# Kernel optimization log

Hardware: AMD Instinct MI355X
Metric: run time of the kernel (lower is better)

The kernel has to match this reference:

```python
import jax, jax.numpy as jnp
import numpy as np

K1 = 3                      # spline kernel size per pseudo dim
SIZE = float(np.sqrt(2.0))  # pseudo_cartesian normalization size


def spline_weights(p, k):
    """Degree-1 open B-spline basis over 2D pseudo coords.
    p: [..., 2] in [0,1]. Returns basis [..., 4], weight_index [..., 4]."""
    v = jnp.clip(p, 0.0, 1.0) * (k - 1)
    lo = jnp.floor(v)
    frac = v - lo
    lo = lo.astype(jnp.int32)
    off = jnp.array([0, 1], dtype=jnp.int32)
    w0 = jnp.stack([1.0 - frac[..., 0], frac[..., 0]], axis=-1)   # [...,2]
    w1 = jnp.stack([1.0 - frac[..., 1], frac[..., 1]], axis=-1)   # [...,2]
    i0 = jnp.clip(lo[..., 0:1] + off, 0, k - 1)                    # [...,2]
    i1 = jnp.clip(lo[..., 1:2] + off, 0, k - 1)                    # [...,2]
    basis = (w0[..., :, None] * w1[..., None, :]).reshape(*p.shape[:-1], 4)
    widx = (i0[..., :, None] + k * i1[..., None, :]).reshape(*p.shape[:-1], 4)
    return basis, widx


def setup_inputs() -> dict:
    key = jax.random.key(0)
    kx, ke, kp, kq, kw, kb = jax.random.split(key, 6)
    N, C, P, E, K = 50000, 64, 16, 800000, K1 * K1
    x = jax.random.normal(kx, (N, C), dtype=jnp.float32)
    pos = jax.random.uniform(kp, (N, 2), dtype=jnp.float32)
    pose = jax.random.normal(kq, (N, P, 2), dtype=jnp.float32)
    pose = pose / (jnp.linalg.norm(pose, axis=-1, keepdims=True) + 1e-8)  # unit pose vectors
    W = jax.random.normal(kw, (P, K, C), dtype=jnp.float32) / np.sqrt(C * 4.0)
    bias = jax.random.normal(kb, (P,), dtype=jnp.float32) * 0.01
    edge_index = jax.random.randint(ke, (2, E), 0, N, dtype=jnp.int64)
    return {"x": x, "pos": pos, "pose": pose, "W": W, "bias": bias,
            "edge_index": edge_index}


def reference(x, pos, pose, W, bias, edge_index):
    N, C = x.shape
    P = pose.shape[1]
    row, col = edge_index[0], edge_index[1]
    # pseudo_cartesian: normalized relative position in [0,1]^2
    pseudo = (pos[col] - pos[row]) / (2.0 * SIZE) + 0.5              # [E,2]
    # posevec_to_rotmat on detached pose vectors
    pose_c = jax.lax.stop_gradient(pose)
    a, b = pose_c[..., 0], pose_c[..., 1]
    R = jnp.stack([jnp.stack([a, -b], -1), jnp.stack([b, a], -1)], -2)  # [N,P,2,2]
    Re = R[row]                                                      # [E,P,2,2]
    # rotate pseudo coords about (0.5, 0.5), batched over all poses
    p = jnp.einsum('epij,ej->epi', Re, pseudo - 0.5) + 0.5           # [E,P,2]
    basis, widx = spline_weights(p, K1)                              # [E,P,4]
    # SplineConv (out_channels=1, no root weight, no norm):
    # precompute per-node per-pose per-kernel-bin projections
    Z = jnp.einsum('nc,pkc->npk', x, W)                              # [N,P,K]
    pidx = jnp.arange(P)[None, :, None]
    vals = Z[col[:, None, None], pidx, widx]                         # [E,P,4]
    msg = jnp.sum(basis * vals, axis=-1)                             # [E,P]
    out = jax.ops.segment_sum(msg, row, num_segments=N)              # [N,P]
    return out + bias[None, :]
```

## Files before the change

kernel.cpp:

```cpp
#include <hip/hip_runtime.h>

#define C_DIM 64
#define P_DIM 16
#define K_DIM 9
#define ZROW 10
#define ZNODE (P_DIM * ZROW)
#define NT 10
#define WELEM (160 * C_DIM)
#define INV2S 0.35355339059327373f

typedef __attribute__((ext_vector_type(8))) short short8v;
typedef __attribute__((ext_vector_type(4))) float f32x4;
typedef uint uint4a __attribute__((ext_vector_type(4), aligned(4)));

__device__ __forceinline__ ushort f2bf(float f) {
    uint u = __builtin_bit_cast(uint, f);
    return (ushort)((u + 0x7FFFu + ((u >> 16) & 1u)) >> 16);
}
__device__ __forceinline__ float bf2f(ushort h) {
    return __builtin_bit_cast(float, ((uint)h) << 16);
}

__global__ __launch_bounds__(256) void prep_kernel(const float* __restrict__ W,
                                                   const float* __restrict__ pose,
                                                   const float* __restrict__ bias,
                                                   float* __restrict__ out,
                                                   ushort* __restrict__ Whi,
                                                   ushort* __restrict__ Wlo,
                                                   uint* __restrict__ pose_bf,
                                                   int N) {
    const int g = blockIdx.x * 256 + threadIdx.x;
    const int gsz = gridDim.x * 256;

    if (g < WELEM / 2) {
        const int j  = g >> 5;
        const int k2 = g & 31;
        const int p  = j / 10;
        const int k  = j - p * 10;
        float2 w2 = make_float2(0.0f, 0.0f);
        if (k < 9) w2 = ((const float2*)W)[(p * 9 + k) * (C_DIM / 2) + k2];
        const ushort h0 = f2bf(w2.x);
        const ushort h1 = f2bf(w2.y);
        ((uint*)Whi)[g] = (uint)h0 | ((uint)h1 << 16);
        ((uint*)Wlo)[g] = (uint)f2bf(w2.x - bf2f(h0)) |
                          ((uint)f2bf(w2.y - bf2f(h1)) << 16);
    }

    if (pose_bf != nullptr) {
        for (int i = g; i < N * P_DIM; i += gsz) {
            const float2 ab = ((const float2*)pose)[i];
            pose_bf[i] = (uint)f2bf(ab.x) | ((uint)f2bf(ab.y) << 16);
        }
    }

    {
        const float4 b4 = ((const float4*)bias)[g & 3];
        for (int i = g; i < N * 4; i += gsz) ((float4*)out)[i] = b4;
    }
}

__global__ __launch_bounds__(256) void z_gemm_kernel(const float* __restrict__ x,
                                                     const ushort* __restrict__ Whi,
                                                     const ushort* __restrict__ Wlo,
                                                     ushort* __restrict__ Zb,
                                                     int N) {
    __shared__ ushort w_hi[WELEM];
    __shared__ ushort w_lo[WELEM];

    const int tid = threadIdx.x;
    const int block_row = blockIdx.x * 64;

    for (int i = tid; i < 160 * 16; i += 256) {
        const uint4 vh = ((const uint4*)Whi)[i];
        const uint4 vl = ((const uint4*)Wlo)[i];
        const int lin = i * 8;
        const int j   = lin >> 6;
        const int w   = lin & 63;
        const int swz = j * 64 + (w ^ ((j & 7) << 3));
        *(uint4*)&w_hi[swz] = vh;
        *(uint4*)&w_lo[swz] = vl;
    }
    __syncthreads();

    const int lane = tid & 63;
    const int wv   = tid >> 6;
    const int col  = lane & 15;
    const int kg   = lane >> 4;

    const int arow = block_row + wv * 16 + col;
    const float* xr = x + (size_t)(arow < N ? arow : 0) * C_DIM;
    float4 x0 = ((const float4*)xr)[kg * 2];
    float4 x1 = ((const float4*)xr)[kg * 2 + 1];
    float4 x2 = ((const float4*)xr)[8 + kg * 2];
    float4 x3 = ((const float4*)xr)[8 + kg * 2 + 1];
    if (arow >= N) {
        x0 = x1 = x2 = x3 = make_float4(0.f, 0.f, 0.f, 0.f);
    }

    short8v a_hi0, a_lo0, a_hi1, a_lo1;
    {
        const float t0[8] = {x0.x, x0.y, x0.z, x0.w, x1.x, x1.y, x1.z, x1.w};
        const float t1[8] = {x2.x, x2.y, x2.z, x2.w, x3.x, x3.y, x3.z, x3.w};
        #pragma unroll
        for (int e = 0; e < 8; ++e) {
            const ushort h = f2bf(t0[e]);
            a_hi0[e] = (short)h;
            a_lo0[e] = (short)f2bf(t0[e] - bf2f(h));
            const ushort g = f2bf(t1[e]);
            a_hi1[e] = (short)g;
            a_lo1[e] = (short)f2bf(t1[e] - bf2f(g));
        }
    }

    const int orow0 = block_row + wv * 16 + kg * 4;

    #pragma unroll
    for (int nt = 0; nt < NT; ++nt) {
        const int j  = nt * 16 + col;
        const int sx = (j & 7) << 3;
        const int b0off = j * 64 + ((kg * 8) ^ sx);
        const int b1off = j * 64 + ((32 + kg * 8) ^ sx);
        const short8v bh0 = *(const short8v*)&w_hi[b0off];
        const short8v bh1 = *(const short8v*)&w_hi[b1off];
        const short8v bl0 = *(const short8v*)&w_lo[b0off];
        const short8v bl1 = *(const short8v*)&w_lo[b1off];

        f32x4 acc = {0.f, 0.f, 0.f, 0.f};
        acc = __builtin_amdgcn_mfma_f32_16x16x32_bf16(a_lo0, bh0, acc, 0, 0, 0);
        acc = __builtin_amdgcn_mfma_f32_16x16x32_bf16(a_hi0, bl0, acc, 0, 0, 0);
        acc = __builtin_amdgcn_mfma_f32_16x16x32_bf16(a_lo1, bh1, acc, 0, 0, 0);
        acc = __builtin_amdgcn_mfma_f32_16x16x32_bf16(a_hi1, bl1, acc, 0, 0, 0);
        acc = __builtin_amdgcn_mfma_f32_16x16x32_bf16(a_hi0, bh0, acc, 0, 0, 0);
        acc = __builtin_amdgcn_mfma_f32_16x16x32_bf16(a_hi1, bh1, acc, 0, 0, 0);

        #pragma unroll
        for (int r = 0; r < 4; ++r) {
            const int row = orow0 + r;
            if (row < N) Zb[(size_t)row * ZNODE + j] = f2bf(acc[r]);
        }
    }
}

#define EILP 8
template <bool USEBF>
__global__ __launch_bounds__(256) void edge_kernel(const int* __restrict__ ei,
                                                   const float* __restrict__ pos,
                                                   const float* __restrict__ pose,
                                                   const uint* __restrict__ pose_bf,
                                                   const ushort* __restrict__ Zb,
                                                   float* __restrict__ out,
                                                   int E) {
    const int p  = threadIdx.x & 15;
    const int eg = threadIdx.x >> 4;
    const int e0 = blockIdx.x * (16 * EILP) + eg;

    int  r[EILP], c[EILP];
    bool valid[EILP];
    #pragma unroll
    for (int it = 0; it < EILP; ++it) {
        int e = e0 + it * 16;
        valid[it] = (e < E);
        int ec = valid[it] ? e : 0;
        r[it] = ei[ec];
        c[it] = ei[E + ec];
    }

    float d0[EILP], d1[EILP];
    #pragma unroll
    for (int it = 0; it < EILP; ++it) {
        const float2 pc = ((const float2*)pos)[c[it]];
        const float2 pr = ((const float2*)pos)[r[it]];
        d0[it] = (pc.x - pr.x) * INV2S;
        d1[it] = (pc.y - pr.y) * INV2S;
    }

    float a_[EILP], b_[EILP];
    #pragma unroll
    for (int it = 0; it < EILP; ++it) {
        if (USEBF) {
            const uint ab = pose_bf[(size_t)r[it] * P_DIM + p];
            a_[it] = bf2f((ushort)(ab & 0xffffu));
            b_[it] = bf2f((ushort)(ab >> 16));
        } else {
            const float2 ab = ((const float2*)pose)[(size_t)r[it] * P_DIM + p];
            a_[it] = ab.x;
            b_[it] = ab.y;
        }
    }

    uint4a qv[EILP];
    uint   q4[EILP];
    #pragma unroll
    for (int it = 0; it < EILP; ++it) {
        const uint* Zp = (const uint*)(Zb + (size_t)c[it] * ZNODE) + p * (ZROW / 2);
        qv[it] = *(const uint4a*)Zp;
        q4[it] = Zp[4];
    }

    #pragma unroll
    for (int it = 0; it < EILP; ++it) {
        const float p0 = fmaf(a_[it], d0[it], fmaf(-b_[it], d1[it], 0.5f));
        const float p1 = fmaf(b_[it], d0[it], fmaf( a_[it], d1[it], 0.5f));

        const float v0 = fminf(fmaxf(p0, 0.0f), 1.0f) * 2.0f;
        const float v1 = fminf(fmaxf(p1, 0.0f), 1.0f) * 2.0f;
        const bool b0 = (v0 >= 1.0f);
        const bool b1 = (v1 >= 1.0f);
        const float f0 = v0 - (b0 ? 1.0f : 0.0f);
        const float f1 = v1 - (b1 ? 1.0f : 0.0f);

        const uint A0 = qv[it][0], A1 = qv[it][1], A2 = qv[it][2],
                   A3 = qv[it][3], A4 = q4[it];
        const uint W0 = b1 ? ((A1 >> 16) | (A2 << 16)) : A0;
        const uint W1 = b1 ? ((A2 >> 16) | (A3 << 16)) : A1;
        const uint W2 = b1 ? ((A3 >> 16) | (A4 << 16)) : A2;
        const uint s = b0 ? 16u : 0u;
        const float z00 = bf2f((ushort)(W0 >> s));
        const float z10 = bf2f((ushort)(b0 ? (W1 & 0xffffu) : (W0 >> 16)));
        const float z01 = bf2f((ushort)(b0 ? (W2 & 0xffffu) : (W1 >> 16)));
        const float z11 = bf2f((ushort)(W2 >> s));

        const float w00 = (1.0f - f0) * (1.0f - f1);
        const float w01 = (1.0f - f0) * f1;
        const float w10 = f0 * (1.0f - f1);
        const float w11 = f0 * f1;

        float m = w00 * z00;
        m = fmaf(w01, z01, m);
        m = fmaf(w10, z10, m);
        m = fmaf(w11, z11, m);

        if (valid[it]) atomicAdd(&out[(size_t)r[it] * P_DIM + p], m);
    }
}

extern "C" void kernel_launch(void* const* d_in, const int* in_sizes, int n_in,
                              void* d_out, int out_size, void* d_ws, size_t ws_size,
                              hipStream_t stream) {
    const float* x    = (const float*)d_in[0];
    const float* pos  = (const float*)d_in[1];
    const float* pose = (const float*)d_in[2];
    const float* W    = (const float*)d_in[3];
    const float* bias = (const float*)d_in[4];
    const int*   ei   = (const int*)d_in[5];

    const int N = in_sizes[0] / C_DIM;
    const int E = in_sizes[5] / 2;

    float* out = (float*)d_out;

    ushort* Whi = (ushort*)d_ws;
    ushort* Wlo = Whi + WELEM;
    ushort* Zb  = Wlo + WELEM;

    const size_t w_bytes    = (size_t)2 * WELEM * sizeof(ushort);
    const size_t zb_bytes   = (size_t)N * ZNODE * sizeof(ushort);
    const size_t pose_bytes = (size_t)N * P_DIM * sizeof(uint);
    uint* pose_bf = (ws_size >= w_bytes + zb_bytes + pose_bytes)
                        ? (uint*)((char*)Zb + zb_bytes) : nullptr;

    prep_kernel<<<3200, 256, 0, stream>>>(W, pose, bias, out, Whi, Wlo, pose_bf, N);
    z_gemm_kernel<<<(N + 63) / 64, 256, 0, stream>>>(x, Whi, Wlo, Zb, N);

    const int eblocks = (E + 16 * EILP - 1) / (16 * EILP);
    if (pose_bf != nullptr)
        edge_kernel<true><<<eblocks, 256, 0, stream>>>(ei, pos, pose, pose_bf, Zb, out, E);
    else
        edge_kernel<false><<<eblocks, 256, 0, stream>>>(ei, pos, pose, pose_bf, Zb, out, E);
}
```

Measured before the change: 144.5 us.

## Fuse prep, GEMM and edge kernels into one cooperative persistent kernel

Merges the three separate launches (prep/bias init, Z GEMM, edge scatter) into a single cooperative kernel with grid-wide syncs between phases and grid-stride loops over GEMM tiles and edge batches. The aim is to remove launch gaps and tail effects between kernels and to stage the weight tables into LDS once per persistent block rather than once per GEMM block. In exchange, the grid is fixed at 1024 (or 512) blocks with launch_bounds(256,4), grid.sync adds barrier cost, and occupancy and latency hiding in the edge phase may be lower than with the original large grid. The three-kernel path is kept as a fallback if the cooperative launch fails.

```diff
diff --git a/kernel.cpp b/kernel.cpp
--- a/kernel.cpp
+++ b/kernel.cpp
@@ -1,4 +1,7 @@
 #include <hip/hip_runtime.h>
+#include <hip/hip_cooperative_groups.h>
+
+namespace cg = cooperative_groups;
 
 #define C_DIM 64
 #define P_DIM 16
@@ -7,6 +10,7 @@
 #define ZNODE (P_DIM * ZROW)
 #define NT 10
 #define WELEM (160 * C_DIM)
+#define EILP 8
 #define INV2S 0.35355339059327373f
 
 typedef __attribute__((ext_vector_type(8))) short short8v;
@@ -21,55 +25,44 @@
     return __builtin_bit_cast(float, ((uint)h) << 16);
 }
 
-__global__ __launch_bounds__(256) void prep_kernel(const float* __restrict__ W,
-                                                   const float* __restrict__ pose,
-                                                   const float* __restrict__ bias,
-                                                   float* __restrict__ out,
-                                                   ushort* __restrict__ Whi,
-                                                   ushort* __restrict__ Wlo,
-                                                   uint* __restrict__ pose_bf,
-                                                   int N) {
-    const int g = blockIdx.x * 256 + threadIdx.x;
-    const int gsz = gridDim.x * 256;
-
-    if (g < WELEM / 2) {
-        const int j  = g >> 5;
-        const int k2 = g & 31;
+template <bool USEBF>
+__device__ __forceinline__ void do_prep(int gt, int G,
+                                        const float* __restrict__ W,
+                                        const float* __restrict__ pose,
+                                        const float* __restrict__ bias,
+                                        float* __restrict__ out,
+                                        ushort* __restrict__ Whi,
+                                        ushort* __restrict__ Wlo,
+                                        uint* __restrict__ pose_bf, int N) {
+    if (gt < WELEM / 2) {
+        const int j  = gt >> 5;
+        const int k2 = gt & 31;
         const int p  = j / 10;
         const int k  = j - p * 10;
         float2 w2 = make_float2(0.0f, 0.0f);
         if (k < 9) w2 = ((const float2*)W)[(p * 9 + k) * (C_DIM / 2) + k2];
         const ushort h0 = f2bf(w2.x);
         const ushort h1 = f2bf(w2.y);
-        ((uint*)Whi)[g] = (uint)h0 | ((uint)h1 << 16);
-        ((uint*)Wlo)[g] = (uint)f2bf(w2.x - bf2f(h0)) |
-                          ((uint)f2bf(w2.y - bf2f(h1)) << 16);
-    }
-
-    if (pose_bf != nullptr) {
-        for (int i = g; i < N * P_DIM; i += gsz) {
+        ((uint*)Whi)[gt] = (uint)h0 | ((uint)h1 << 16);
+        ((uint*)Wlo)[gt] = (uint)f2bf(w2.x - bf2f(h0)) |
+                           ((uint)f2bf(w2.y - bf2f(h1)) << 16);
+    }
+    if (USEBF) {
+        for (int i = gt; i < N * P_DIM; i += G) {
             const float2 ab = ((const float2*)pose)[i];
             pose_bf[i] = (uint)f2bf(ab.x) | ((uint)f2bf(ab.y) << 16);
         }
     }
-
     {
-        const float4 b4 = ((const float4*)bias)[g & 3];
-        for (int i = g; i < N * 4; i += gsz) ((float4*)out)[i] = b4;
-    }
-}
-
-__global__ __launch_bounds__(256) void z_gemm_kernel(const float* __restrict__ x,
-                                                     const ushort* __restrict__ Whi,
-                                                     const ushort* __restrict__ Wlo,
-                                                     ushort* __restrict__ Zb,
-                                                     int N) {
-    __shared__ ushort w_hi[WELEM];
-    __shared__ ushort w_lo[WELEM];
-
-    const int tid = threadIdx.x;
-    const int block_row = blockIdx.x * 64;
-
+        const float4 b4 = ((const float4*)bias)[gt & 3];
+        for (int i = gt; i < N * 4; i += G) ((float4*)out)[i] = b4;
+    }
+}
+
+__device__ __forceinline__ void stage_tables(int tid,
+                                             const ushort* __restrict__ Whi,
+                                             const ushort* __restrict__ Wlo,
+                                             ushort* w_hi, ushort* w_lo) {
     for (int i = tid; i < 160 * 16; i += 256) {
         const uint4 vh = ((const uint4*)Whi)[i];
         const uint4 vl = ((const uint4*)Wlo)[i];
@@ -80,8 +73,13 @@
         *(uint4*)&w_hi[swz] = vh;
         *(uint4*)&w_lo[swz] = vl;
     }
-    __syncthreads();
-
+}
+
+__device__ __forceinline__ void gemm_tile(int tile, int tid,
+                                          const float* __restrict__ x,
+                                          ushort* __restrict__ Zb, int N,
+                                          const ushort* w_hi, const ushort* w_lo) {
+    const int block_row = tile * 64;
     const int lane = tid & 63;
     const int wv   = tid >> 6;
     const int col  = lane & 15;
@@ -141,18 +139,17 @@
     }
 }
 
-#define EILP 8
-template <bool USEBF>
-__global__ __launch_bounds__(256) void edge_kernel(const int* __restrict__ ei,
-                                                   const float* __restrict__ pos,
-                                                   const float* __restrict__ pose,
-                                                   const uint* __restrict__ pose_bf,
-                                                   const ushort* __restrict__ Zb,
-                                                   float* __restrict__ out,
-                                                   int E) {
-    const int p  = threadIdx.x & 15;
-    const int eg = threadIdx.x >> 4;
-    const int e0 = blockIdx.x * (16 * EILP) + eg;
+template <bool USEBF>
+__device__ __forceinline__ void edge_batch(int b, int tid,
+                                           const int* __restrict__ ei,
+                                           const float* __restrict__ pos,
+                                           const float* __restrict__ pose,
+                                           const uint* __restrict__ pose_bf,
+                                           const ushort* __restrict__ Zb,
+                                           float* __restrict__ out, int E) {
+    const int p  = tid & 15;
+    const int eg = tid >> 4;
+    const int e0 = b * (16 * EILP) + eg;
 
     int  r[EILP], c[EILP];
     bool valid[EILP];
@@ -234,6 +231,77 @@
     }
 }
 
+template <bool USEBF>
+__global__ __launch_bounds__(256, 4) void fused_kernel(const float* __restrict__ x,
+                                                       const float* __restrict__ pos,
+                                                       const float* __restrict__ pose,
+                                                       const float* __restrict__ W,
+                                                       const float* __restrict__ bias,
+                                                       const int* __restrict__ ei,
+                                                       float* __restrict__ out,
+                                                       ushort* __restrict__ Whi,
+                                                       ushort* __restrict__ Wlo,
+                                                       ushort* __restrict__ Zb,
+                                                       uint* __restrict__ pose_bf,
+                                                       int N, int E) {
+    __shared__ ushort w_hi[WELEM];
+    __shared__ ushort w_lo[WELEM];
+    cg::grid_group grid = cg::this_grid();
+
+    const int tid = threadIdx.x;
+    const int gt  = blockIdx.x * 256 + tid;
+    const int G   = gridDim.x * 256;
+
+    do_prep<USEBF>(gt, G, W, pose, bias, out, Whi, Wlo, pose_bf, N);
+    __threadfence();
+    grid.sync();
+
+    stage_tables(tid, Whi, Wlo, w_hi, w_lo);
+    __syncthreads();
+    const int ntiles = (N + 63) / 64;
+    for (int t = blockIdx.x; t < ntiles; t += gridDim.x)
+        gemm_tile(t, tid, x, Zb, N, w_hi, w_lo);
+    __threadfence();
+    grid.sync();
+
+    const int nb = (E + 16 * EILP - 1) / (16 * EILP);
+    for (int b = blockIdx.x; b < nb; b += gridDim.x)
+        edge_batch<USEBF>(b, tid, ei, pos, pose, pose_bf, Zb, out, E);
+}
+
+template <bool USEBF>
+__global__ __launch_bounds__(256) void prep_kernel(const float* __restrict__ W,
+                                                   const float* __restrict__ pose,
+                                                   const float* __restrict__ bias,
+                                                   float* __restrict__ out,
+                                                   ushort* __restrict__ Whi,
+                                                   ushort* __restrict__ Wlo,
+                                                   uint* __restrict__ pose_bf, int N) {
+    do_prep<USEBF>(blockIdx.x * 256 + threadIdx.x, gridDim.x * 256,
+                   W, pose, bias, out, Whi, Wlo, pose_bf, N);
+}
+
+__global__ __launch_bounds__(256) void z_gemm_kernel(const float* __restrict__ x,
+                                                     const ushort* __restrict__ Whi,
+                                                     const ushort* __restrict__ Wlo,
+                                                     ushort* __restrict__ Zb, int N) {
+    __shared__ ushort w_hi[WELEM];
+    __shared__ ushort w_lo[WELEM];
+    stage_tables(threadIdx.x, Whi, Wlo, w_hi, w_lo);
+    __syncthreads();
+    gemm_tile(blockIdx.x, threadIdx.x, x, Zb, N, w_hi, w_lo);
+}
+
+template <bool USEBF>
+__global__ __launch_bounds__(256) void edge_kernel(const int* __restrict__ ei,
+                                                   const float* __restrict__ pos,
+                                                   const float* __restrict__ pose,
+                                                   const uint* __restrict__ pose_bf,
+                                                   const ushort* __restrict__ Zb,
+                                                   float* __restrict__ out, int E) {
+    edge_batch<USEBF>(blockIdx.x, threadIdx.x, ei, pos, pose, pose_bf, Zb, out, E);
+}
+
 extern "C" void kernel_launch(void* const* d_in, const int* in_sizes, int n_in,
                               void* d_out, int out_size, void* d_ws, size_t ws_size,
                               hipStream_t stream) {
@@ -259,9 +327,25 @@
     uint* pose_bf = (ws_size >= w_bytes + zb_bytes + pose_bytes)
                         ? (uint*)((char*)Zb + zb_bytes) : nullptr;
 
-    prep_kernel<<<3200, 256, 0, stream>>>(W, pose, bias, out, Whi, Wlo, pose_bf, N);
+    void* args[] = {(void*)&x, (void*)&pos, (void*)&pose, (void*)&W,
+                    (void*)&bias, (void*)&ei, (void*)&out, (void*)&Whi,
+                    (void*)&Wlo, (void*)&Zb, (void*)&pose_bf,
+                    (void*)&N, (void*)&E};
+    const void* fk = (pose_bf != nullptr)
+                         ? (const void*)&fused_kernel<true>
+                         : (const void*)&fused_kernel<false>;
+    hipError_t err = hipLaunchCooperativeKernel(fk, dim3(1024), dim3(256),
+                                                args, 0, stream);
+    if (err != hipSuccess)
+        err = hipLaunchCooperativeKernel(fk, dim3(512), dim3(256),
+                                         args, 0, stream);
+    if (err == hipSuccess) return;
+
+    if (pose_bf != nullptr)
+        prep_kernel<true><<<3200, 256, 0, stream>>>(W, pose, bias, out, Whi, Wlo, pose_bf, N);
+    else
+        prep_kernel<false><<<3200, 256, 0, stream>>>(W, pose, bias, out, Whi, Wlo, pose_bf, N);
     z_gemm_kernel<<<(N + 63) / 64, 256, 0, stream>>>(x, Whi, Wlo, Zb, N);
-
     const int eblocks = (E + 16 * EILP - 1) / (16 * EILP);
     if (pose_bf != nullptr)
         edge_kernel<true><<<eblocks, 256, 0, stream>>>(ei, pos, pose, pose_bf, Zb, out, E);
```

Result: slower. 563.7 us (+290.0%).
